# Kernel tuning notes

Hardware: AMD Instinct MI355X
Metric: run time of the kernel (lower is better)

The kernel has to match this reference:

```python
import jax, jax.numpy as jnp
import numpy as np

N_NODES = 50000
N_EDGES = 800000
D_IN, D_HID, D_OUT = 128, 256, 128


def setup_inputs() -> dict:
    key = jax.random.key(0)
    ks = jax.random.split(key, 8)
    x = jax.random.normal(ks[0], (N_NODES, D_IN), dtype=jnp.float32)
    edge_src = jax.random.randint(ks[1], (N_EDGES,), 0, N_NODES, dtype=jnp.int32)
    edge_dst = jnp.sort(jax.random.randint(ks[2], (N_EDGES,), 0, N_NODES, dtype=jnp.int32))
    edge_val = jax.random.uniform(ks[3], (N_EDGES,), dtype=jnp.float32)
    eps = jnp.zeros((1,), dtype=jnp.float32)
    w1 = jax.random.normal(ks[4], (D_IN, D_HID), dtype=jnp.float32) * (1.0 / np.sqrt(D_IN))
    b1 = jnp.zeros((D_HID,), dtype=jnp.float32)
    w2 = jax.random.normal(ks[5], (D_HID, D_OUT), dtype=jnp.float32) * (1.0 / np.sqrt(D_HID))
    b2 = jnp.zeros((D_OUT,), dtype=jnp.float32)
    return {"x": x, "edge_src": edge_src, "edge_dst": edge_dst, "edge_val": edge_val,
            "eps": eps, "w1": w1, "b1": b1, "w2": w2, "b2": b2}


def reference(x, edge_src, edge_dst, edge_val, eps, w1, b1, w2, b2):
    # Sparse adjacency aggregation: (A @ x)[i] = sum_{e: dst=i} val_e * x[src_e]
    msgs = edge_val[:, None] * x[edge_src]            # [E, D_IN]
    agg = jax.ops.segment_sum(msgs, edge_dst, num_segments=N_NODES)  # [N, D_IN]
    h = agg + (1.0 + eps[0]) * x                      # AX + (1+eps)X
    # 2-layer MLP
    h = jax.nn.relu(h @ w1 + b1)                      # [N, D_HID]
    out = h @ w2 + b2                                 # [N, D_OUT]
    return out
```

## Files before the change

### kernel.cpp

```cpp
#include <hip/hip_runtime.h>
#include <hip/hip_bf16.h>
#include <cstdint>
#include <type_traits>

#define N_NODES 50000
#define N_EDGES 800000
#define D_IN 128
#define D_HID 256
#define D_OUT 128

typedef __bf16 bf16;
typedef __bf16 bf16x8 __attribute__((ext_vector_type(8)));
typedef __bf16 bf16x4 __attribute__((ext_vector_type(4)));
typedef float f32x4 __attribute__((ext_vector_type(4)));

__global__ __launch_bounds__(256) void prep_kernel(
    const float* __restrict__ x, const float* __restrict__ eps,
    const float* __restrict__ w1, const float* __restrict__ w2,
    bf16* __restrict__ aggb, bf16* __restrict__ xb,
    bf16* __restrict__ w1t, bf16* __restrict__ w2t) {
  const int i = blockIdx.x * 256 + threadIdx.x;
  const float scale = 1.0f + eps[0];
  float4 v = ((const float4*)x)[i];
  ((bf16x4*)xb)[i] = bf16x4{(bf16)v.x, (bf16)v.y, (bf16)v.z, (bf16)v.w};
  ((bf16x4*)aggb)[i] = bf16x4{(bf16)(v.x * scale), (bf16)(v.y * scale),
                              (bf16)(v.z * scale), (bf16)(v.w * scale)};
  if (i < D_IN * D_HID) {
    int k = i >> 8, n = i & 255;
    w1t[n * D_IN + k] = (bf16)w1[i];
  } else if (i < 2 * D_IN * D_HID) {
    int j = i - D_IN * D_HID;
    int k = j >> 7, n = j & 127;
    w2t[n * D_HID + k] = (bf16)w2[j];
  }
}

__device__ __forceinline__ void flush_pk(bf16* __restrict__ agg, int node,
                                         int lane, float2 acc) {
  union { struct { bf16 x, y; } h; int i; } u;
  u.h.x = (bf16)acc.x; u.h.y = (bf16)acc.y;
  const bf16* p = &agg[(long)node * D_IN + lane * 2];
  asm volatile("global_atomic_pk_add_bf16 %0, %1, off"
               :: "v"(p), "v"(u.i) : "memory");
}

__global__ __launch_bounds__(256) void edge_agg_kernel(
    const bf16* __restrict__ xb, const int* __restrict__ src,
    const int* __restrict__ dst, const float* __restrict__ val,
    bf16* __restrict__ agg) {
  const int wave = (blockIdx.x << 2) | (threadIdx.x >> 6);
  const int lane = threadIdx.x & 63;
  const int e0 = __builtin_amdgcn_readfirstlane(wave << 6);

  float2 acc = make_float2(0.f, 0.f);
  int cur = dst[e0];

  #pragma unroll 1
  for (int j = 0; j < 64; j += 16) {
    int s[16], d[16];
    float v[16];
    #pragma unroll
    for (int t = 0; t < 16; ++t) {
      s[t] = src[e0 + j + t];
      d[t] = dst[e0 + j + t];
      v[t] = val[e0 + j + t];
    }
    int g[16];
    #pragma unroll
    for (int t = 0; t < 16; ++t)
      g[t] = *(const int*)&xb[(long)s[t] * D_IN + lane * 2];
    #pragma unroll
    for (int t = 0; t < 16; ++t) {
      if (d[t] != cur) {
        flush_pk(agg, cur, lane, acc);
        acc.x = 0.f; acc.y = 0.f;
        cur = d[t];
      }
      float gx = __uint_as_float((unsigned)g[t] << 16);
      float gy = __uint_as_float((unsigned)g[t] & 0xffff0000u);
      acc.x = fmaf(v[t], gx, acc.x);
      acc.y = fmaf(v[t], gy, acc.y);
    }
  }
  flush_pk(agg, cur, lane, acc);
}

template <int KDIM, int NOUT, bool RELU, typename TC>
__global__ __launch_bounds__(256) void gemm(
    const bf16* __restrict__ A, const bf16* __restrict__ Wt,
    const float* __restrict__ bias, TC* __restrict__ C) {
  constexpr int LDL = 136;
  __shared__ alignas(16) bf16 As[64][LDL];
  __shared__ alignas(16) bf16 Bs[64][LDL];

  const int tid = threadIdx.x;
  const int m0 = blockIdx.x * 64;
  const int n0 = blockIdx.y * 64;
  const int wave = tid >> 6;
  const int lane = tid & 63;
  const int wm = (wave >> 1) * 32;
  const int wn = (wave & 1) * 32;
  const int l15 = lane & 15;
  const int quad = lane >> 4;

  f32x4 acc[2][2] = {};

  for (int kt = 0; kt < KDIM; kt += 128) {
    #pragma unroll
    for (int it = 0; it < 4; ++it) {
      int idx = tid + it * 256;
      int r = idx >> 4;
      int c8 = (idx & 15) << 3;
      int row = m0 + r; if (row >= N_NODES) row = N_NODES - 1;
      *(bf16x8*)&As[r][c8] = *(const bf16x8*)&A[(long)row * KDIM + kt + c8];
    }
    #pragma unroll
    for (int it = 0; it < 4; ++it) {
      int idx = tid + it * 256;
      int r = idx >> 4;
      int c8 = (idx & 15) << 3;
      *(bf16x8*)&Bs[r][c8] = *(const bf16x8*)&Wt[(long)(n0 + r) * KDIM + kt + c8];
    }
    __syncthreads();

    #pragma unroll
    for (int ks = 0; ks < 4; ++ks) {
      int kq = ks * 32 + quad * 8;
      bf16x8 a0 = *(const bf16x8*)&As[wm + l15][kq];
      bf16x8 a1 = *(const bf16x8*)&As[wm + 16 + l15][kq];
      bf16x8 b0 = *(const bf16x8*)&Bs[wn + l15][kq];
      bf16x8 b1 = *(const bf16x8*)&Bs[wn + 16 + l15][kq];
      acc[0][0] = __builtin_amdgcn_mfma_f32_16x16x32_bf16(a0, b0, acc[0][0], 0, 0, 0);
      acc[0][1] = __builtin_amdgcn_mfma_f32_16x16x32_bf16(a0, b1, acc[0][1], 0, 0, 0);
      acc[1][0] = __builtin_amdgcn_mfma_f32_16x16x32_bf16(a1, b0, acc[1][0], 0, 0, 0);
      acc[1][1] = __builtin_amdgcn_mfma_f32_16x16x32_bf16(a1, b1, acc[1][1], 0, 0, 0);
    }
    __syncthreads();
  }

  #pragma unroll
  for (int mf = 0; mf < 2; ++mf) {
    #pragma unroll
    for (int nf = 0; nf < 2; ++nf) {
      int col = n0 + wn + nf * 16 + l15;
      float bv = bias[col];
      #pragma unroll
      for (int r = 0; r < 4; ++r) {
        int row = m0 + wm + mf * 16 + quad * 4 + r;
        if (row < N_NODES) {
          float vv = acc[mf][nf][r] + bv;
          if constexpr (RELU) vv = fmaxf(vv, 0.f);
          if constexpr (std::is_same_v<TC, float>)
            C[(long)row * NOUT + col] = vv;
          else
            C[(long)row * NOUT + col] = (bf16)vv;
        }
      }
    }
  }
}

extern "C" void kernel_launch(void* const* d_in, const int* in_sizes, int n_in,
                              void* d_out, int out_size, void* d_ws, size_t ws_size,
                              hipStream_t stream) {
  const float* x    = (const float*)d_in[0];
  const int*   esrc = (const int*)d_in[1];
  const int*   edst = (const int*)d_in[2];
  const float* evl  = (const float*)d_in[3];
  const float* eps  = (const float*)d_in[4];
  const float* w1   = (const float*)d_in[5];
  const float* b1   = (const float*)d_in[6];
  const float* w2   = (const float*)d_in[7];
  const float* b2   = (const float*)d_in[8];
  float* out = (float*)d_out;

  bf16* aggb = (bf16*)d_ws;
  bf16* xb   = aggb + (size_t)N_NODES * D_IN;
  bf16* h    = xb + (size_t)N_NODES * D_IN;
  bf16* w1t  = h + (size_t)N_NODES * D_HID;
  bf16* w2t  = w1t + D_IN * D_HID;

  prep_kernel<<<(N_NODES * D_IN / 4) / 256, 256, 0, stream>>>(
      x, eps, w1, w2, aggb, xb, w1t, w2t);
  edge_agg_kernel<<<N_EDGES / 256, 256, 0, stream>>>(xb, esrc, edst, evl, aggb);
  gemm<D_IN, D_HID, true, bf16>
      <<<dim3((N_NODES + 63) / 64, D_HID / 64), 256, 0, stream>>>(aggb, w1t, b1, h);
  gemm<D_HID, D_OUT, false, float>
      <<<dim3((N_NODES + 63) / 64, D_OUT / 64), 256, 0, stream>>>(h, w2t, b2, out);
}
```

Measured before the change: 155.3 us.

## Build CSR offsets, aggregate per node without atomics, fuse both MLP GEMMs

Builds CSR row offsets from the sorted destination array and switches edge aggregation to one wave per node, which removes bf16 atomics and folds the (1+eps)x term into the same pass. The two GEMM launches are merged into one kernel that keeps the hidden activations in shared memory and the weight fragments in registers, so the hidden matrix is never written to or read back from global memory. In exchange it adds a CSR-building launch, gives the aggregation uneven per-wave work because node degrees vary, and raises register pressure in the fused MLP kernel.

```diff
diff --git a/kernel.cpp b/kernel.cpp
--- a/kernel.cpp
+++ b/kernel.cpp
@@ -1,7 +1,6 @@
 #include <hip/hip_runtime.h>
 #include <hip/hip_bf16.h>
 #include <cstdint>
-#include <type_traits>
 
 #define N_NODES 50000
 #define N_EDGES 800000
@@ -15,16 +14,12 @@
 typedef float f32x4 __attribute__((ext_vector_type(4)));
 
 __global__ __launch_bounds__(256) void prep_kernel(
-    const float* __restrict__ x, const float* __restrict__ eps,
+    const float* __restrict__ x,
     const float* __restrict__ w1, const float* __restrict__ w2,
-    bf16* __restrict__ aggb, bf16* __restrict__ xb,
-    bf16* __restrict__ w1t, bf16* __restrict__ w2t) {
+    bf16* __restrict__ xb, bf16* __restrict__ w1t, bf16* __restrict__ w2t) {
   const int i = blockIdx.x * 256 + threadIdx.x;
-  const float scale = 1.0f + eps[0];
   float4 v = ((const float4*)x)[i];
   ((bf16x4*)xb)[i] = bf16x4{(bf16)v.x, (bf16)v.y, (bf16)v.z, (bf16)v.w};
-  ((bf16x4*)aggb)[i] = bf16x4{(bf16)(v.x * scale), (bf16)(v.y * scale),
-                              (bf16)(v.z * scale), (bf16)(v.w * scale)};
   if (i < D_IN * D_HID) {
     int k = i >> 8, n = i & 255;
     w1t[n * D_IN + k] = (bf16)w1[i];
@@ -35,128 +30,161 @@
   }
 }
 
-__device__ __forceinline__ void flush_pk(bf16* __restrict__ agg, int node,
-                                         int lane, float2 acc) {
-  union { struct { bf16 x, y; } h; int i; } u;
-  u.h.x = (bf16)acc.x; u.h.y = (bf16)acc.y;
-  const bf16* p = &agg[(long)node * D_IN + lane * 2];
-  asm volatile("global_atomic_pk_add_bf16 %0, %1, off"
-               :: "v"(p), "v"(u.i) : "memory");
-}
-
-__global__ __launch_bounds__(256) void edge_agg_kernel(
+__global__ __launch_bounds__(256) void csr_kernel(
+    const int* __restrict__ dst, int* __restrict__ offs) {
+  const int e = blockIdx.x * 256 + threadIdx.x;
+  if (e >= N_EDGES) return;
+  const int b = dst[e];
+  const int a = (e == 0) ? -1 : dst[e - 1];
+  for (int n = a + 1; n <= b; ++n) offs[n] = e;
+  if (e == N_EDGES - 1)
+    for (int n = b + 1; n <= N_NODES; ++n) offs[n] = N_EDGES;
+}
+
+__global__ __launch_bounds__(256) void node_agg_kernel(
     const bf16* __restrict__ xb, const int* __restrict__ src,
-    const int* __restrict__ dst, const float* __restrict__ val,
-    bf16* __restrict__ agg) {
-  const int wave = (blockIdx.x << 2) | (threadIdx.x >> 6);
+    const float* __restrict__ val, const int* __restrict__ offs,
+    const float* __restrict__ eps, bf16* __restrict__ aggb) {
+  const int node = __builtin_amdgcn_readfirstlane(
+      (blockIdx.x << 2) | (threadIdx.x >> 6));
   const int lane = threadIdx.x & 63;
-  const int e0 = __builtin_amdgcn_readfirstlane(wave << 6);
+  const int s = __builtin_amdgcn_readfirstlane(offs[node]);
+  const int e = __builtin_amdgcn_readfirstlane(offs[node + 1]);
 
   float2 acc = make_float2(0.f, 0.f);
-  int cur = dst[e0];
-
-  #pragma unroll 1
-  for (int j = 0; j < 64; j += 16) {
-    int s[16], d[16];
-    float v[16];
-    #pragma unroll
-    for (int t = 0; t < 16; ++t) {
-      s[t] = src[e0 + j + t];
-      d[t] = dst[e0 + j + t];
-      v[t] = val[e0 + j + t];
-    }
-    int g[16];
-    #pragma unroll
-    for (int t = 0; t < 16; ++t)
-      g[t] = *(const int*)&xb[(long)s[t] * D_IN + lane * 2];
-    #pragma unroll
-    for (int t = 0; t < 16; ++t) {
-      if (d[t] != cur) {
-        flush_pk(agg, cur, lane, acc);
-        acc.x = 0.f; acc.y = 0.f;
-        cur = d[t];
-      }
+  int i = s;
+  for (; i + 8 <= e; i += 8) {
+    int sv[8]; float vv[8]; int g[8];
+    #pragma unroll
+    for (int t = 0; t < 8; ++t) { sv[t] = src[i + t]; vv[t] = val[i + t]; }
+    #pragma unroll
+    for (int t = 0; t < 8; ++t)
+      g[t] = *(const int*)&xb[(long)sv[t] * D_IN + lane * 2];
+    #pragma unroll
+    for (int t = 0; t < 8; ++t) {
       float gx = __uint_as_float((unsigned)g[t] << 16);
       float gy = __uint_as_float((unsigned)g[t] & 0xffff0000u);
-      acc.x = fmaf(v[t], gx, acc.x);
-      acc.y = fmaf(v[t], gy, acc.y);
+      acc.x = fmaf(vv[t], gx, acc.x);
+      acc.y = fmaf(vv[t], gy, acc.y);
     }
   }
-  flush_pk(agg, cur, lane, acc);
-}
-
-template <int KDIM, int NOUT, bool RELU, typename TC>
-__global__ __launch_bounds__(256) void gemm(
-    const bf16* __restrict__ A, const bf16* __restrict__ Wt,
-    const float* __restrict__ bias, TC* __restrict__ C) {
-  constexpr int LDL = 136;
-  __shared__ alignas(16) bf16 As[64][LDL];
-  __shared__ alignas(16) bf16 Bs[64][LDL];
+  for (; i < e; ++i) {
+    int sv = src[i]; float vv = val[i];
+    int g = *(const int*)&xb[(long)sv * D_IN + lane * 2];
+    acc.x = fmaf(vv, __uint_as_float((unsigned)g << 16), acc.x);
+    acc.y = fmaf(vv, __uint_as_float((unsigned)g & 0xffff0000u), acc.y);
+  }
+
+  const float scale = 1.0f + eps[0];
+  int xg = *(const int*)&xb[(long)node * D_IN + lane * 2];
+  acc.x = fmaf(scale, __uint_as_float((unsigned)xg << 16), acc.x);
+  acc.y = fmaf(scale, __uint_as_float((unsigned)xg & 0xffff0000u), acc.y);
+
+  union { struct { bf16 x, y; } h; int i_; } u;
+  u.h.x = (bf16)acc.x; u.h.y = (bf16)acc.y;
+  *(int*)&aggb[(long)node * D_IN + lane * 2] = u.i_;
+}
+
+__global__ __launch_bounds__(256) void mlp_fused(
+    const bf16* __restrict__ A, const bf16* __restrict__ W1t,
+    const bf16* __restrict__ W2t, const float* __restrict__ b1,
+    const float* __restrict__ b2, float* __restrict__ out) {
+  constexpr int LDA = 136;
+  constexpr int LDH = 264;
+  __shared__ alignas(16) bf16 As[64][LDA];
+  __shared__ alignas(16) bf16 Hs[64][LDH];
 
   const int tid = threadIdx.x;
   const int m0 = blockIdx.x * 64;
-  const int n0 = blockIdx.y * 64;
   const int wave = tid >> 6;
   const int lane = tid & 63;
-  const int wm = (wave >> 1) * 32;
-  const int wn = (wave & 1) * 32;
   const int l15 = lane & 15;
   const int quad = lane >> 4;
 
-  f32x4 acc[2][2] = {};
-
-  for (int kt = 0; kt < KDIM; kt += 128) {
-    #pragma unroll
-    for (int it = 0; it < 4; ++it) {
-      int idx = tid + it * 256;
-      int r = idx >> 4;
-      int c8 = (idx & 15) << 3;
-      int row = m0 + r; if (row >= N_NODES) row = N_NODES - 1;
-      *(bf16x8*)&As[r][c8] = *(const bf16x8*)&A[(long)row * KDIM + kt + c8];
-    }
-    #pragma unroll
-    for (int it = 0; it < 4; ++it) {
-      int idx = tid + it * 256;
-      int r = idx >> 4;
-      int c8 = (idx & 15) << 3;
-      *(bf16x8*)&Bs[r][c8] = *(const bf16x8*)&Wt[(long)(n0 + r) * KDIM + kt + c8];
-    }
-    __syncthreads();
-
-    #pragma unroll
-    for (int ks = 0; ks < 4; ++ks) {
-      int kq = ks * 32 + quad * 8;
-      bf16x8 a0 = *(const bf16x8*)&As[wm + l15][kq];
-      bf16x8 a1 = *(const bf16x8*)&As[wm + 16 + l15][kq];
-      bf16x8 b0 = *(const bf16x8*)&Bs[wn + l15][kq];
-      bf16x8 b1 = *(const bf16x8*)&Bs[wn + 16 + l15][kq];
-      acc[0][0] = __builtin_amdgcn_mfma_f32_16x16x32_bf16(a0, b0, acc[0][0], 0, 0, 0);
-      acc[0][1] = __builtin_amdgcn_mfma_f32_16x16x32_bf16(a0, b1, acc[0][1], 0, 0, 0);
-      acc[1][0] = __builtin_amdgcn_mfma_f32_16x16x32_bf16(a1, b0, acc[1][0], 0, 0, 0);
-      acc[1][1] = __builtin_amdgcn_mfma_f32_16x16x32_bf16(a1, b1, acc[1][1], 0, 0, 0);
-    }
-    __syncthreads();
-  }
-
-  #pragma unroll
-  for (int mf = 0; mf < 2; ++mf) {
-    #pragma unroll
-    for (int nf = 0; nf < 2; ++nf) {
-      int col = n0 + wn + nf * 16 + l15;
-      float bv = bias[col];
+  #pragma unroll
+  for (int it = 0; it < 4; ++it) {
+    int idx = tid + it * 256;
+    int r = idx >> 4;
+    int c8 = (idx & 15) << 3;
+    int row = m0 + r; if (row >= N_NODES) row = N_NODES - 1;
+    *(bf16x8*)&As[r][c8] = *(const bf16x8*)&A[(long)row * D_IN + c8];
+  }
+
+  bf16x8 w1f[4][4];
+  #pragma unroll
+  for (int nf = 0; nf < 4; ++nf) {
+    int n = wave * 64 + nf * 16 + l15;
+    #pragma unroll
+    for (int ks = 0; ks < 4; ++ks)
+      w1f[nf][ks] = *(const bf16x8*)&W1t[(long)n * D_IN + ks * 32 + quad * 8];
+  }
+  __syncthreads();
+
+  f32x4 acc[4][4] = {};
+  #pragma unroll
+  for (int ks = 0; ks < 4; ++ks) {
+    int kq = ks * 32 + quad * 8;
+    bf16x8 a[4];
+    #pragma unroll
+    for (int mf = 0; mf < 4; ++mf)
+      a[mf] = *(const bf16x8*)&As[mf * 16 + l15][kq];
+    #pragma unroll
+    for (int mf = 0; mf < 4; ++mf)
+      #pragma unroll
+      for (int nf = 0; nf < 4; ++nf)
+        acc[mf][nf] = __builtin_amdgcn_mfma_f32_16x16x32_bf16(
+            a[mf], w1f[nf][ks], acc[mf][nf], 0, 0, 0);
+  }
+
+  #pragma unroll
+  for (int nf = 0; nf < 4; ++nf) {
+    int col = wave * 64 + nf * 16 + l15;
+    float bv = b1[col];
+    #pragma unroll
+    for (int mf = 0; mf < 4; ++mf)
+      #pragma unroll
+      for (int r = 0; r < 4; ++r)
+        Hs[mf * 16 + quad * 4 + r][col] = (bf16)fmaxf(acc[mf][nf][r] + bv, 0.f);
+  }
+
+  bf16x8 w2f[2][8];
+  #pragma unroll
+  for (int nf2 = 0; nf2 < 2; ++nf2) {
+    int n = wave * 32 + nf2 * 16 + l15;
+    #pragma unroll
+    for (int ks2 = 0; ks2 < 8; ++ks2)
+      w2f[nf2][ks2] = *(const bf16x8*)&W2t[(long)n * D_HID + ks2 * 32 + quad * 8];
+  }
+  __syncthreads();
+
+  f32x4 acc2[4][2] = {};
+  #pragma unroll
+  for (int ks2 = 0; ks2 < 8; ++ks2) {
+    int kq = ks2 * 32 + quad * 8;
+    bf16x8 ha[4];
+    #pragma unroll
+    for (int mf = 0; mf < 4; ++mf)
+      ha[mf] = *(const bf16x8*)&Hs[mf * 16 + l15][kq];
+    #pragma unroll
+    for (int mf = 0; mf < 4; ++mf)
+      #pragma unroll
+      for (int nf2 = 0; nf2 < 2; ++nf2)
+        acc2[mf][nf2] = __builtin_amdgcn_mfma_f32_16x16x32_bf16(
+            ha[mf], w2f[nf2][ks2], acc2[mf][nf2], 0, 0, 0);
+  }
+
+  #pragma unroll
+  for (int nf2 = 0; nf2 < 2; ++nf2) {
+    int col = wave * 32 + nf2 * 16 + l15;
+    float bv = b2[col];
+    #pragma unroll
+    for (int mf = 0; mf < 4; ++mf)
       #pragma unroll
       for (int r = 0; r < 4; ++r) {
-        int row = m0 + wm + mf * 16 + quad * 4 + r;
-        if (row < N_NODES) {
-          float vv = acc[mf][nf][r] + bv;
-          if constexpr (RELU) vv = fmaxf(vv, 0.f);
-          if constexpr (std::is_same_v<TC, float>)
-            C[(long)row * NOUT + col] = vv;
-          else
-            C[(long)row * NOUT + col] = (bf16)vv;
-        }
+        int row = m0 + mf * 16 + quad * 4 + r;
+        if (row < N_NODES)
+          out[(long)row * D_OUT + col] = acc2[mf][nf2][r] + bv;
       }
-    }
   }
 }
 
@@ -176,15 +204,15 @@
 
   bf16* aggb = (bf16*)d_ws;
   bf16* xb   = aggb + (size_t)N_NODES * D_IN;
-  bf16* h    = xb + (size_t)N_NODES * D_IN;
-  bf16* w1t  = h + (size_t)N_NODES * D_HID;
+  bf16* w1t  = xb + (size_t)N_NODES * D_IN;
   bf16* w2t  = w1t + D_IN * D_HID;
+  int*  offs = (int*)(w2t + D_HID * D_OUT);
 
   prep_kernel<<<(N_NODES * D_IN / 4) / 256, 256, 0, stream>>>(
-      x, eps, w1, w2, aggb, xb, w1t, w2t);
-  edge_agg_kernel<<<N_EDGES / 256, 256, 0, stream>>>(xb, esrc, edst, evl, aggb);
-  gemm<D_IN, D_HID, true, bf16>
-      <<<dim3((N_NODES + 63) / 64, D_HID / 64), 256, 0, stream>>>(aggb, w1t, b1, h);
-  gemm<D_HID, D_OUT, false, float>
-      <<<dim3((N_NODES + 63) / 64, D_OUT / 64), 256, 0, stream>>>(h, w2t, b2, out);
-}
+      x, w1, w2, xb, w1t, w2t);
+  csr_kernel<<<(N_EDGES + 255) / 256, 256, 0, stream>>>(edst, offs);
+  node_agg_kernel<<<(N_NODES + 3) / 4, 256, 0, stream>>>(
+      xb, esrc, evl, offs, eps, aggb);
+  mlp_fused<<<(N_NODES + 63) / 64, 256, 0, stream>>>(
+      aggb, w1t, w2t, b1, b2, out);
+}
```

After: 156.1 us. No clear change (+0.5%).
